# Performance work log

Measured on AMD Instinct MI355X. Metric: run time of the kernel, lower is better.

## Reference

```python
import jax, jax.numpy as jnp
import numpy as np

N = 50000      # nodes
E = 600000     # edges
B = 256        # graphs in batch
F_IN = 128     # num_features
H = 128        # nhid
D = 3 * H      # Set2Set in_channels (concat of 3 conv outputs)
C = 10         # num_classes
STEPS = 10     # Set2Set processing steps


def setup_inputs() -> dict:
    key = jax.random.key(0)
    ks = jax.random.split(key, 24)

    def gn(k, shape, fan_in):
        return jax.random.normal(k, shape, dtype=jnp.float32) / jnp.sqrt(jnp.float32(fan_in))

    x = jax.random.normal(ks[0], (N, F_IN), dtype=jnp.float32)
    edge_index = jax.random.randint(ks[1], (2, E), 0, N, dtype=jnp.int32)
    # sorted graph-assignment covering all B segments
    batch = (jnp.arange(N, dtype=jnp.int32) * B) // N

    inp = dict(x=x, edge_index=edge_index, batch=batch)
    # GraphConv params: out = x @ W_root + aggr(x_j) @ W_rel + b
    inp["W1_root"] = gn(ks[2], (F_IN, H), F_IN)
    inp["W1_rel"] = gn(ks[3], (F_IN, H), F_IN)
    inp["b1"] = jnp.zeros((H,), jnp.float32)
    inp["W2_root"] = gn(ks[4], (H, H), H)
    inp["W2_rel"] = gn(ks[5], (H, H), H)
    inp["b2"] = jnp.zeros((H,), jnp.float32)
    inp["W3_root"] = gn(ks[6], (H, H), H)
    inp["W3_rel"] = gn(ks[7], (H, H), H)
    inp["b3"] = jnp.zeros((H,), jnp.float32)
    # Set2Set LSTM: input 2*D, hidden D, gate order i,f,g,o
    inp["W_ih"] = gn(ks[8], (4 * D, 2 * D), 2 * D)
    inp["W_hh"] = gn(ks[9], (4 * D, D), D)
    inp["b_ih"] = jnp.zeros((4 * D,), jnp.float32)
    inp["b_hh"] = jnp.zeros((4 * D,), jnp.float32)
    # MLP head
    inp["lin1_W"] = gn(ks[10], (2 * D, H), 2 * D)
    inp["lin1_b"] = jnp.zeros((H,), jnp.float32)
    inp["lin2_W"] = gn(ks[11], (H, H // 2), H)
    inp["lin2_b"] = jnp.zeros((H // 2,), jnp.float32)
    inp["lin3_W"] = gn(ks[12], (H // 2, C), H // 2)
    inp["lin3_b"] = jnp.zeros((C,), jnp.float32)
    return inp


def _graph_conv(x, src, dst, W_root, W_rel, b):
    # sum_{j in N(i)} x_j, then linear; plus root transform
    agg = jax.ops.segment_sum(x[src], dst, num_segments=N)  # [N, F]
    return jax.nn.relu(x @ W_root + agg @ W_rel + b)


def _segment_softmax(e, seg, num):
    m = jax.ops.segment_max(e, seg, num_segments=num)
    ex = jnp.exp(e - m[seg])
    den = jax.ops.segment_sum(ex, seg, num_segments=num)
    return ex / den[seg]


def _set2set(x, batch, W_ih, W_hh, b_ih, b_hh):
    # x: [N, D], returns [B, 2D]
    q_star = jnp.zeros((B, 2 * D), x.dtype)
    h = jnp.zeros((B, D), x.dtype)
    c = jnp.zeros((B, D), x.dtype)
    for _ in range(STEPS):
        gates = q_star @ W_ih.T + b_ih + h @ W_hh.T + b_hh  # [B, 4D]
        i, f, g, o = jnp.split(gates, 4, axis=-1)
        i, f, o = jax.nn.sigmoid(i), jax.nn.sigmoid(f), jax.nn.sigmoid(o)
        c = f * c + i * jnp.tanh(g)
        h = o * jnp.tanh(c)
        q = h                                              # [B, D]
        e = jnp.sum(x * q[batch], axis=-1)                 # [N]
        a = _segment_softmax(e, batch, B)                  # [N]
        r = jax.ops.segment_sum(a[:, None] * x, batch, num_segments=B)  # [B, D]
        q_star = jnp.concatenate([q, r], axis=-1)
    return q_star


def reference(x, edge_index, batch,
              W1_root, W1_rel, b1, W2_root, W2_rel, b2, W3_root, W3_rel, b3,
              W_ih, W_hh, b_ih, b_hh,
              lin1_W, lin1_b, lin2_W, lin2_b, lin3_W, lin3_b):
    src, dst = edge_index[0], edge_index[1]
    x1 = _graph_conv(x, src, dst, W1_root, W1_rel, b1)
    x2 = _graph_conv(x1, src, dst, W2_root, W2_rel, b2)
    x3 = _graph_conv(x2, src, dst, W3_root, W3_rel, b3)
    xc = jnp.concatenate([x1, x2, x3], axis=1)             # [N, 3H]
    p = _set2set(xc, batch, W_ih, W_hh, b_ih, b_hh)        # [B, 6H]
    h1 = jax.nn.relu(p @ lin1_W + lin1_b)
    # dropout p=0.5 is identity in eval mode
    h2 = jax.nn.relu(h1 @ lin2_W + lin2_b)
    return jax.nn.log_softmax(h2 @ lin3_W + lin3_b, axis=-1)
```

## Files before the change

kernel.cpp:

```cpp
#include <hip/hip_runtime.h>
#include <hip/hip_bf16.h>
#include <cstddef>

constexpr int NN = 50000;
constexpr int EE = 600000;
constexpr int BBg = 256;

typedef __attribute__((ext_vector_type(8))) short short8;
typedef __attribute__((ext_vector_type(4))) float f32x4;

__device__ __forceinline__ unsigned short bf16_rne(float f) {
    unsigned int u = __float_as_uint(f);
    unsigned int r = u + 0x7fffu + ((u >> 16) & 1u);
    return (unsigned short)(r >> 16);
}
__device__ __forceinline__ float bf16_tof(unsigned short h) {
    return __uint_as_float(((unsigned int)h) << 16);
}

__global__ __launch_bounds__(256) void bake_bimg(
    const float* __restrict__ Wr1, const float* __restrict__ Wl1,
    const float* __restrict__ Wr2, const float* __restrict__ Wl2,
    const float* __restrict__ Wr3, const float* __restrict__ Wl3,
    unsigned short* __restrict__ bimg)
{
    int t = blockIdx.x * 256 + threadIdx.x;
    const int kp = t % 384;
    int rest = t / 384;
    const int c = rest & 63;  rest >>= 6;
    const int cb = rest & 3;  rest >>= 2;
    const int l = rest;
    const int kk = kp & 127;
    const int gc = cb * 64 + c;
    const float* W;
    if (gc < 128) W = (l == 0) ? Wr1 : (l == 1) ? Wr2 : Wr3;
    else          W = (l == 0) ? Wl1 : (l == 1) ? Wl2 : Wl3;
    const float v = W[kk * 128 + (gc & 127)];
    const unsigned short hi = bf16_rne(v);
    unsigned short out = hi;
    if (kp >= 256) out = bf16_rne(v - bf16_tof(hi));
    const int e = (c * 384 + kp) ^ ((c & 7) << 3);
    bimg[(l * 4 + cb) * 24576 + e] = out;
}

__global__ __launch_bounds__(256) void prep_x2(const float* __restrict__ x,
                                               unsigned short* __restrict__ x2)
{
    const int t = blockIdx.x * 256 + threadIdx.x;
    if (t >= NN * 128) return;
    const int n = t >> 7, k = t & 127;
    const float v = x[t];
    const unsigned short hi = bf16_rne(v);
    x2[(size_t)n * 256 + k] = hi;
    x2[(size_t)n * 256 + 128 + k] = bf16_rne(v - bf16_tof(hi));
}

__global__ __launch_bounds__(256) void bake_wt2(const float* __restrict__ w_ih,
                                                const float* __restrict__ w_hh,
                                                unsigned short* __restrict__ wt2)
{
    const int t = blockIdx.x * 256 + threadIdx.x;
    const int o = t & 7;
    const int j = (t >> 3) % 1536;
    const int rest = (t >> 3) / 1536;
    const int kg = rest % 96;
    const int v = rest / 96;
    const int k = kg * 8 + o;
    float val = w_ih[(size_t)j * 768 + k];
    if (k < 384) val += w_hh[(size_t)j * 384 + k];
    const unsigned short hi = bf16_rne(val);
    wt2[t] = v ? bf16_rne(val - bf16_tof(hi)) : hi;
}

__global__ __launch_bounds__(256) void conv_mfma(
    const unsigned short* __restrict__ x2,
    const unsigned short* __restrict__ bimg,
    float* __restrict__ tu,
    const float* __restrict__ bias)
{
    __shared__ unsigned short Bt[24576];
    const int tid = threadIdx.x;
    const int cb = blockIdx.x;
    const int rBase = blockIdx.y * 128;

    {
        const unsigned short* src = bimg + cb * 24576;
#pragma unroll
        for (int i = 0; i < 12; ++i) {
            const int e = (tid + i * 256) * 8;
            *(uint4*)&Bt[e] = *(const uint4*)&src[e];
        }
    }
    __syncthreads();

    const int lane = tid & 63;
    const int w = tid >> 6;
    const int r0w = rBase + w * 32;
    const int l15 = lane & 15;
    const int kg = lane >> 4;

    f32x4 acc[2][4];
#pragma unroll
    for (int rf = 0; rf < 2; ++rf)
#pragma unroll
        for (int cf = 0; cf < 4; ++cf) acc[rf][cf] = (f32x4){0.f, 0.f, 0.f, 0.f};

    const int rr0 = r0w + l15;
    const int rr1 = r0w + 16 + l15;
    const unsigned short* arow0 = x2 + (size_t)(rr0 < NN ? rr0 : NN - 1) * 256 + kg * 8;
    const unsigned short* arow1 = x2 + (size_t)(rr1 < NN ? rr1 : NN - 1) * 256 + kg * 8;

#pragma unroll
    for (int s = 0; s < 12; ++s) {
        const int acol = (s < 8 ? s : s - 8) * 32;
        const short8 a0 = *(const short8*)(arow0 + acol);
        const short8 a1 = *(const short8*)(arow1 + acol);
        short8 bfr[4];
#pragma unroll
        for (int cf = 0; cf < 4; ++cf) {
            const int c = cf * 16 + l15;
            const int e = (c * 384 + s * 32 + kg * 8) ^ ((c & 7) << 3);
            bfr[cf] = *(const short8*)&Bt[e];
        }
#pragma unroll
        for (int cf = 0; cf < 4; ++cf) {
            acc[0][cf] = __builtin_amdgcn_mfma_f32_16x16x32_bf16(a0, bfr[cf], acc[0][cf], 0, 0, 0);
            acc[1][cf] = __builtin_amdgcn_mfma_f32_16x16x32_bf16(a1, bfr[cf], acc[1][cf], 0, 0, 0);
        }
    }
    const int c0 = cb * 64;
#pragma unroll
    for (int rf = 0; rf < 2; ++rf) {
#pragma unroll
        for (int reg = 0; reg < 4; ++reg) {
            const int grow = r0w + rf * 16 + kg * 4 + reg;
            if (grow < NN) {
#pragma unroll
                for (int cf = 0; cf < 4; ++cf) {
                    const int gc = c0 + cf * 16 + l15;
                    float v = acc[rf][cf][reg];
                    if (gc < 128) v += bias[gc];
                    tu[(size_t)grow * 256 + gc] = v;
                }
            }
        }
    }
}

__global__ __launch_bounds__(256) void gates_mfma(
    const unsigned short* __restrict__ qh2,
    const unsigned short* __restrict__ wt2,
    float* __restrict__ gpart)
{
    const int tid = threadIdx.x;
    const int lane = tid & 63;
    const int w = tid >> 6;
    const int c0 = blockIdx.x * 64;
    const int r0w = blockIdx.y * 128 + w * 32;
    const int p = blockIdx.z;
    const int l15 = lane & 15;
    const int kg = lane >> 4;

    f32x4 acc[2][4];
#pragma unroll
    for (int rf = 0; rf < 2; ++rf)
#pragma unroll
        for (int cf = 0; cf < 4; ++cf) acc[rf][cf] = (f32x4){0.f, 0.f, 0.f, 0.f};

    const int abase = (p == 1) ? 768 : 0;
    const unsigned short* arow0 = qh2 + (size_t)(r0w + l15) * 1536 + abase + kg * 8;
    const unsigned short* arow1 = arow0 + 16 * 1536;
    const unsigned short* bbase = wt2 + (p == 2 ? 1179648 : 0)
                                + (size_t)(kg * 1536 + c0 + l15) * 8;

#pragma unroll 4
    for (int km = 0; km < 24; ++km) {
        const short8 a0 = *(const short8*)(arow0 + km * 32);
        const short8 a1 = *(const short8*)(arow1 + km * 32);
#pragma unroll
        for (int cf = 0; cf < 4; ++cf) {
            const short8 bf = *(const short8*)(bbase + (size_t)km * 4 * 1536 * 8 + cf * 128);
            acc[0][cf] = __builtin_amdgcn_mfma_f32_16x16x32_bf16(a0, bf, acc[0][cf], 0, 0, 0);
            acc[1][cf] = __builtin_amdgcn_mfma_f32_16x16x32_bf16(a1, bf, acc[1][cf], 0, 0, 0);
        }
    }
    float* gout = gpart + (size_t)p * 393216;
#pragma unroll
    for (int rf = 0; rf < 2; ++rf)
#pragma unroll
        for (int reg = 0; reg < 4; ++reg) {
            const int grow = r0w + rf * 16 + kg * 4 + reg;
#pragma unroll
            for (int cf = 0; cf < 4; ++cf)
                gout[(size_t)grow * 1536 + c0 + cf * 16 + l15] = acc[rf][cf][reg];
        }
}

__global__ __launch_bounds__(256) void deg_hist(const int* __restrict__ ei,
                                                int* __restrict__ deg)
{
    const int e = blockIdx.x * 256 + threadIdx.x;
    if (e < EE) atomicAdd(&deg[ei[EE + e]], 1);
}

__global__ __launch_bounds__(256) void scan1(const int* __restrict__ deg,
                                             int* __restrict__ tmp_ex,
                                             int* __restrict__ bsum)
{
    __shared__ int s[256];
    const int i = blockIdx.x * 256 + threadIdx.x;
    const int v = (i < NN) ? deg[i] : 0;
    s[threadIdx.x] = v;
    __syncthreads();
#pragma unroll
    for (int off = 1; off < 256; off <<= 1) {
        const int t = (threadIdx.x >= off) ? s[threadIdx.x - off] : 0;
        __syncthreads();
        s[threadIdx.x] += t;
        __syncthreads();
    }
    tmp_ex[i] = s[threadIdx.x] - v;
    if (threadIdx.x == 255) bsum[blockIdx.x] = s[255];
}

__global__ __launch_bounds__(256) void scan2(const int* __restrict__ bsum,
                                             int* __restrict__ boff)
{
    __shared__ int s[256];
    const int v = (threadIdx.x < 196) ? bsum[threadIdx.x] : 0;
    s[threadIdx.x] = v;
    __syncthreads();
#pragma unroll
    for (int off = 1; off < 256; off <<= 1) {
        const int t = (threadIdx.x >= off) ? s[threadIdx.x - off] : 0;
        __syncthreads();
        s[threadIdx.x] += t;
        __syncthreads();
    }
    if (threadIdx.x < 196) boff[threadIdx.x] = s[threadIdx.x] - v;
}

__global__ __launch_bounds__(256) void scan3(const int* __restrict__ tmp_ex,
                                             const int* __restrict__ boff,
                                             int* __restrict__ rowptr,
                                             int* __restrict__ cursor)
{
    const int i = blockIdx.x * 256 + threadIdx.x;
    if (i < NN) {
        const int r = tmp_ex[i] + boff[blockIdx.x];
        rowptr[i] = r;
        cursor[i] = r;
    }
    if (i == 0) rowptr[NN] = EE;
}

__global__ __launch_bounds__(256) void scatter_edges(const int* __restrict__ ei,
                                                     int* __restrict__ cursor,
                                                     int* __restrict__ col)
{
    const int e = blockIdx.x * 256 + threadIdx.x;
    if (e >= EE) return;
    const int slot = atomicAdd(&cursor[ei[EE + e]], 1);
    col[slot] = ei[e];
}

__global__ __launch_bounds__(256) void agg_relu(const int* __restrict__ rowptr,
                                                const int* __restrict__ col,
                                                const float* __restrict__ tu,
                                                float* __restrict__ xc, int coloff,
                                                unsigned short* __restrict__ x2n,
                                                int wsplit)
{
    const int node = blockIdx.x * 4 + (threadIdx.x >> 6);
    if (node >= NN) return;
    const int lane = threadIdx.x & 63;
    const int b = rowptr[node];
    const int e = rowptr[node + 1];
    const float* u = tu + 128 + lane * 2;

    float2 a0 = *(const float2*)&tu[(size_t)node * 256 + lane * 2];
    float2 a1 = make_float2(0.f, 0.f);
    float2 a2 = make_float2(0.f, 0.f);
    float2 a3 = make_float2(0.f, 0.f);

    int j = b;
    for (; j + 8 <= e; j += 8) {
        const int s0 = col[j + 0], s1 = col[j + 1], s2 = col[j + 2], s3 = col[j + 3];
        const int s4 = col[j + 4], s5 = col[j + 5], s6 = col[j + 6], s7 = col[j + 7];
        const float2 v0 = *(const float2*)(u + (size_t)s0 * 256);
        const float2 v1 = *(const float2*)(u + (size_t)s1 * 256);
        const float2 v2 = *(const float2*)(u + (size_t)s2 * 256);
        const float2 v3 = *(const float2*)(u + (size_t)s3 * 256);
        const float2 v4 = *(const float2*)(u + (size_t)s4 * 256);
        const float2 v5 = *(const float2*)(u + (size_t)s5 * 256);
        const float2 v6 = *(const float2*)(u + (size_t)s6 * 256);
        const float2 v7 = *(const float2*)(u + (size_t)s7 * 256);
        a0.x += v0.x; a0.y += v0.y;  a1.x += v1.x; a1.y += v1.y;
        a2.x += v2.x; a2.y += v2.y;  a3.x += v3.x; a3.y += v3.y;
        a0.x += v4.x; a0.y += v4.y;  a1.x += v5.x; a1.y += v5.y;
        a2.x += v6.x; a2.y += v6.y;  a3.x += v7.x; a3.y += v7.y;
    }
    for (; j < e; j += 4) {
        const bool c1 = (j + 1 < e), c2 = (j + 2 < e), c3 = (j + 3 < e);
        const int s0 = col[j];
        const int s1 = col[c1 ? j + 1 : j];
        const int s2 = col[c2 ? j + 2 : j];
        const int s3 = col[c3 ? j + 3 : j];
        const float2 v0 = *(const float2*)(u + (size_t)s0 * 256);
        const float2 v1 = *(const float2*)(u + (size_t)s1 * 256);
        const float2 v2 = *(const float2*)(u + (size_t)s2 * 256);
        const float2 v3 = *(const float2*)(u + (size_t)s3 * 256);
        a0.x += v0.x;              a0.y += v0.y;
        a1.x += c1 ? v1.x : 0.f;   a1.y += c1 ? v1.y : 0.f;
        a2.x += c2 ? v2.x : 0.f;   a2.y += c2 ? v2.y : 0.f;
        a3.x += c3 ? v3.x : 0.f;   a3.y += c3 ? v3.y : 0.f;
    }
    float2 acc;
    acc.x = (a0.x + a1.x) + (a2.x + a3.x);
    acc.y = (a0.y + a1.y) + (a2.y + a3.y);
    acc.x = fmaxf(acc.x, 0.f);
    acc.y = fmaxf(acc.y, 0.f);
    *(float2*)&xc[(size_t)node * 384 + coloff + lane * 2] = acc;

    if (wsplit) {
        const unsigned short h0 = bf16_rne(acc.x);
        const unsigned short h1 = bf16_rne(acc.y);
        const unsigned short l0 = bf16_rne(acc.x - bf16_tof(h0));
        const unsigned short l1 = bf16_rne(acc.y - bf16_tof(h1));
        unsigned short* p = x2n + (size_t)node * 256 + lane * 2;
        *(unsigned int*)p = (unsigned int)h0 | ((unsigned int)h1 << 16);
        *(unsigned int*)(p + 128) = (unsigned int)l0 | ((unsigned int)l1 << 16);
    }
}

__global__ __launch_bounds__(512) void lstm_attn(const float* __restrict__ gpart,
                                                 const float* __restrict__ b_ih,
                                                 const float* __restrict__ b_hh,
                                                 float* __restrict__ cbuf,
                                                 float* __restrict__ qh,
                                                 unsigned short* __restrict__ qh2,
                                                 const float* __restrict__ xc)
{
    const int b = blockIdx.x;
    const int start = (b * NN + BBg - 1) / BBg;
    const int end = ((b + 1) * NN + BBg - 1) / BBg;
    const int cnt = end - start;

    __shared__ float qs[384];
    __shared__ float wm[8], wz[8];
    __shared__ float rp[8][384];

    const int tid = threadIdx.x;
    const int lane = tid & 63;
    const int w = tid >> 6;

    if (tid < 384) {
        const int d = tid;
        const float* g0 = gpart + (size_t)b * 1536;
        const float* g1 = g0 + 393216;
        const float* g2 = g1 + 393216;
        float gi = g0[d]        + g1[d]        + g2[d]        + b_ih[d]        + b_hh[d];
        float gf = g0[384 + d]  + g1[384 + d]  + g2[384 + d]  + b_ih[384 + d]  + b_hh[384 + d];
        float gg = g0[768 + d]  + g1[768 + d]  + g2[768 + d]  + b_ih[768 + d]  + b_hh[768 + d];
        float go = g0[1152 + d] + g1[1152 + d] + g2[1152 + d] + b_ih[1152 + d] + b_hh[1152 + d];
        gi = 1.f / (1.f + expf(-gi));
        gf = 1.f / (1.f + expf(-gf));
        go = 1.f / (1.f + expf(-go));
        const float cc = gf * cbuf[b * 384 + d] + gi * tanhf(gg);
        cbuf[b * 384 + d] = cc;
        const float h = go * tanhf(cc);
        qh[(size_t)b * 768 + d] = h;
        qs[d] = h;
        const unsigned short hi = bf16_rne(h);
        qh2[(size_t)b * 1536 + d] = hi;
        qh2[(size_t)b * 1536 + 768 + d] = bf16_rne(h - bf16_tof(hi));
    }
    __syncthreads();

    float q[6];
#pragma unroll
    for (int j = 0; j < 6; ++j) q[j] = qs[lane + 64 * j];

    float m = -3.4e38f, Z = 0.f;
    float r[6] = {0.f, 0.f, 0.f, 0.f, 0.f, 0.f};
    int i = w;
    for (; i + 56 < cnt; i += 64) {
        float xv[8][6];
#pragma unroll
        for (int k = 0; k < 8; ++k) {
            const float* p = xc + (size_t)(start + i + 8 * k) * 384 + lane;
#pragma unroll
            for (int j = 0; j < 6; ++j) xv[k][j] = p[64 * j];
        }
        float d[8];
#pragma unroll
        for (int k = 0; k < 8; ++k) {
            float dd = 0.f;
#pragma unroll
            for (int j = 0; j < 6; ++j) dd = fmaf(xv[k][j], q[j], dd);
            d[k] = dd;
        }
#pragma unroll
        for (int s = 32; s > 0; s >>= 1) {
#pragma unroll
            for (int k = 0; k < 8; ++k) d[k] += __shfl_xor(d[k], s);
        }
        float mn = m;
#pragma unroll
        for (int k = 0; k < 8; ++k) mn = fmaxf(mn, d[k]);
        const float cs = __expf(m - mn);
        float p8[8];
        float ps = 0.f;
#pragma unroll
        for (int k = 0; k < 8; ++k) { p8[k] = __expf(d[k] - mn); ps += p8[k]; }
        Z = Z * cs + ps;
#pragma unroll
        for (int j = 0; j < 6; ++j) {
            float t = r[j] * cs;
#pragma unroll
            for (int k = 0; k < 8; ++k) t = fmaf(p8[k], xv[k][j], t);
            r[j] = t;
        }
        m = mn;
    }
    for (; i < cnt; i += 8) {
        const float* xr = xc + (size_t)(start + i) * 384 + lane;
        float xv[6], d = 0.f;
#pragma unroll
        for (int j = 0; j < 6; ++j) { xv[j] = xr[64 * j]; d = fmaf(xv[j], q[j], d); }
#pragma unroll
        for (int s = 32; s > 0; s >>= 1) d += __shfl_xor(d, s);
        const float mn = fmaxf(m, d);
        const float cs = __expf(m - mn);
        const float p = __expf(d - mn);
        Z = Z * cs + p;
#pragma unroll
        for (int j = 0; j < 6; ++j) r[j] = fmaf(r[j], cs, p * xv[j]);
        m = mn;
    }
#pragma unroll
    for (int j = 0; j < 6; ++j) rp[w][lane + 64 * j] = r[j];
    if (lane == 0) { wm[w] = m; wz[w] = Z; }
    __syncthreads();

    float M = wm[0];
#pragma unroll
    for (int i2 = 1; i2 < 8; ++i2) M = fmaxf(M, wm[i2]);
    float sc[8];
    float Zt = 0.f;
#pragma unroll
    for (int i2 = 0; i2 < 8; ++i2) { sc[i2] = __expf(wm[i2] - M); Zt += wz[i2] * sc[i2]; }
    const float invZ = 1.f / Zt;
    for (int t = tid; t < 384; t += 512) {
        float rr = 0.f;
#pragma unroll
        for (int i2 = 0; i2 < 8; ++i2) rr = fmaf(rp[i2][t], sc[i2], rr);
        const float val = rr * invZ;
        qh[(size_t)b * 768 + 384 + t] = val;
        const unsigned short hi = bf16_rne(val);
        qh2[(size_t)b * 1536 + 384 + t] = hi;
        qh2[(size_t)b * 1536 + 1152 + t] = bf16_rne(val - bf16_tof(hi));
    }
}

__global__ __launch_bounds__(128) void head(const float* __restrict__ qh,
                                            const float* __restrict__ W1,
                                            const float* __restrict__ bias1,
                                            const float* __restrict__ W2,
                                            const float* __restrict__ b2,
                                            const float* __restrict__ W3,
                                            const float* __restrict__ b3,
                                            float* __restrict__ out)
{
    const int b = blockIdx.x;
    const int tid = threadIdx.x;
    __shared__ float qs[768];
    __shared__ float h1s[128];
    __shared__ float h2s[64];
    __shared__ float lg[10];
    for (int k = tid; k < 768; k += 128) qs[k] = qh[(size_t)b * 768 + k];
    __syncthreads();
    float acc = bias1[tid];
    for (int k = 0; k < 768; ++k) acc = fmaf(qs[k], W1[k * 128 + tid], acc);
    h1s[tid] = fmaxf(acc, 0.f);
    __syncthreads();
    if (tid < 64) {
        float a2 = b2[tid];
        for (int k = 0; k < 128; ++k) a2 = fmaf(h1s[k], W2[k * 64 + tid], a2);
        h2s[tid] = fmaxf(a2, 0.f);
    }
    __syncthreads();
    if (tid < 10) {
        float a = b3[tid];
        for (int k = 0; k < 64; ++k) a = fmaf(h2s[k], W3[k * 10 + tid], a);
        lg[tid] = a;
    }
    __syncthreads();
    if (tid < 10) {
        float mx = lg[0];
        for (int j = 1; j < 10; ++j) mx = fmaxf(mx, lg[j]);
        float s = 0.f;
        for (int j = 0; j < 10; ++j) s += expf(lg[j] - mx);
        out[b * 10 + tid] = lg[tid] - mx - logf(s);
    }
}

extern "C" void kernel_launch(void* const* d_in, const int* in_sizes, int n_in,
                              void* d_out, int out_size, void* d_ws, size_t ws_size,
                              hipStream_t stream)
{
    const float* x     = (const float*)d_in[0];
    const int*   ei    = (const int*)d_in[1];
    const float* W1r   = (const float*)d_in[3];
    const float* W1l   = (const float*)d_in[4];
    const float* b1    = (const float*)d_in[5];
    const float* W2r   = (const float*)d_in[6];
    const float* W2l   = (const float*)d_in[7];
    const float* b2    = (const float*)d_in[8];
    const float* W3r   = (const float*)d_in[9];
    const float* W3l   = (const float*)d_in[10];
    const float* b3    = (const float*)d_in[11];
    const float* W_ih  = (const float*)d_in[12];
    const float* W_hh  = (const float*)d_in[13];
    const float* b_ih  = (const float*)d_in[14];
    const float* b_hh  = (const float*)d_in[15];
    const float* lin1W = (const float*)d_in[16];
    const float* lin1b = (const float*)d_in[17];
    const float* lin2W = (const float*)d_in[18];
    const float* lin2b = (const float*)d_in[19];
    const float* lin3W = (const float*)d_in[20];
    const float* lin3b = (const float*)d_in[21];

    float* ws = (float*)d_ws;
    float* xc    = ws;
    float* tu    = ws + 19200000;
    float* qh    = tu;
    float* cbuf  = tu + 196608;
    unsigned short* qh2 = (unsigned short*)(tu + 294912);
    float* gpart = tu + 491520;
    unsigned short* wt2  = (unsigned short*)(ws + 32000000);
    unsigned short* bimg = (unsigned short*)(ws + 33179648);
    unsigned short* x2   = (unsigned short*)(ws + 33327104);
    int*   ib    = (int*)(ws + 39727104);
    int* deg     = ib;
    int* rowptr  = ib + 50000;
    int* cursor  = ib + 100001;
    int* tmp_ex  = ib + 150001;
    int* bsum    = ib + 200177;
    int* boff    = ib + 200433;
    int* col     = ib + 200689;
    float* out   = (float*)d_out;

    hipMemsetAsync(deg, 0, 50000 * sizeof(int), stream);

    bake_wt2<<<9216, 256, 0, stream>>>(W_ih, W_hh, wt2);
    bake_bimg<<<1152, 256, 0, stream>>>(W1r, W1l, W2r, W2l, W3r, W3l, bimg);
    prep_x2<<<25000, 256, 0, stream>>>(x, x2);

    deg_hist<<<2344, 256, 0, stream>>>(ei, deg);
    scan1<<<196, 256, 0, stream>>>(deg, tmp_ex, bsum);
    scan2<<<1, 256, 0, stream>>>(bsum, boff);
    scan3<<<196, 256, 0, stream>>>(tmp_ex, boff, rowptr, cursor);
    scatter_edges<<<2344, 256, 0, stream>>>(ei, cursor, col);

    const float* biases[3] = {b1, b2, b3};
    for (int l = 0; l < 3; ++l) {
        conv_mfma<<<dim3(4, 391), 256, 0, stream>>>(
            x2, bimg + l * 4 * 24576, tu, biases[l]);
        agg_relu<<<12500, 256, 0, stream>>>(rowptr, col, tu, xc, l * 128,
                                            x2, (l < 2) ? 1 : 0);
    }

    hipMemsetAsync(qh, 0, 491520 * sizeof(float), stream);

    for (int s = 0; s < 10; ++s) {
        gates_mfma<<<dim3(24, 2, 3), 256, 0, stream>>>(qh2, wt2, gpart);
        lstm_attn<<<256, 512, 0, stream>>>(gpart, b_ih, b_hh, cbuf, qh, qh2, xc);
    }

    head<<<256, 128, 0, stream>>>(qh, lin1W, lin1b, lin2W, lin2b,
                                  lin3W, lin3b, out);
}
```

Measured before the change: 789.2 us.

## Fuse Set2Set gate GEMM and attention into one persistent kernel with grid barriers

Replaces the 20 alternating gates_mfma/lstm_attn launches with a single persistent 256-block kernel. Each step runs the gate GEMM work spread over warps 0-2 of 192 blocks, then the LSTM update and attention, with a global atomic barrier between phases. This removes per-step launch overhead and idle gaps. The cost is spin-wait barrier latency, and the scheme relies on all 256 blocks of 512 threads being resident at once, or it deadlocks.

Measured after the change: 1.132 ms. 43.4% more time.

```diff
diff --git a/kernel.cpp b/kernel.cpp
--- a/kernel.cpp
+++ b/kernel.cpp
@@ -16,6 +16,17 @@
 }
 __device__ __forceinline__ float bf16_tof(unsigned short h) {
     return __uint_as_float(((unsigned int)h) << 16);
+}
+
+__device__ __forceinline__ void gbar(unsigned* bar, unsigned target) {
+    __syncthreads();
+    if (threadIdx.x == 0) {
+        __threadfence();
+        atomicAdd(bar, 1u);
+        while (atomicAdd(bar, 0u) < target) __builtin_amdgcn_s_sleep(2);
+        __threadfence();
+    }
+    __syncthreads();
 }
 
 __global__ __launch_bounds__(256) void bake_bimg(
@@ -147,55 +158,6 @@
     }
 }
 
-__global__ __launch_bounds__(256) void gates_mfma(
-    const unsigned short* __restrict__ qh2,
-    const unsigned short* __restrict__ wt2,
-    float* __restrict__ gpart)
-{
-    const int tid = threadIdx.x;
-    const int lane = tid & 63;
-    const int w = tid >> 6;
-    const int c0 = blockIdx.x * 64;
-    const int r0w = blockIdx.y * 128 + w * 32;
-    const int p = blockIdx.z;
-    const int l15 = lane & 15;
-    const int kg = lane >> 4;
-
-    f32x4 acc[2][4];
-#pragma unroll
-    for (int rf = 0; rf < 2; ++rf)
-#pragma unroll
-        for (int cf = 0; cf < 4; ++cf) acc[rf][cf] = (f32x4){0.f, 0.f, 0.f, 0.f};
-
-    const int abase = (p == 1) ? 768 : 0;
-    const unsigned short* arow0 = qh2 + (size_t)(r0w + l15) * 1536 + abase + kg * 8;
-    const unsigned short* arow1 = arow0 + 16 * 1536;
-    const unsigned short* bbase = wt2 + (p == 2 ? 1179648 : 0)
-                                + (size_t)(kg * 1536 + c0 + l15) * 8;
-
-#pragma unroll 4
-    for (int km = 0; km < 24; ++km) {
-        const short8 a0 = *(const short8*)(arow0 + km * 32);
-        const short8 a1 = *(const short8*)(arow1 + km * 32);
-#pragma unroll
-        for (int cf = 0; cf < 4; ++cf) {
-            const short8 bf = *(const short8*)(bbase + (size_t)km * 4 * 1536 * 8 + cf * 128);
-            acc[0][cf] = __builtin_amdgcn_mfma_f32_16x16x32_bf16(a0, bf, acc[0][cf], 0, 0, 0);
-            acc[1][cf] = __builtin_amdgcn_mfma_f32_16x16x32_bf16(a1, bf, acc[1][cf], 0, 0, 0);
-        }
-    }
-    float* gout = gpart + (size_t)p * 393216;
-#pragma unroll
-    for (int rf = 0; rf < 2; ++rf)
-#pragma unroll
-        for (int reg = 0; reg < 4; ++reg) {
-            const int grow = r0w + rf * 16 + kg * 4 + reg;
-#pragma unroll
-            for (int cf = 0; cf < 4; ++cf)
-                gout[(size_t)grow * 1536 + c0 + cf * 16 + l15] = acc[rf][cf][reg];
-        }
-}
-
 __global__ __launch_bounds__(256) void deg_hist(const int* __restrict__ ei,
                                                 int* __restrict__ deg)
 {
@@ -333,133 +295,182 @@
     }
 }
 
-__global__ __launch_bounds__(512) void lstm_attn(const float* __restrict__ gpart,
-                                                 const float* __restrict__ b_ih,
-                                                 const float* __restrict__ b_hh,
-                                                 float* __restrict__ cbuf,
-                                                 float* __restrict__ qh,
-                                                 unsigned short* __restrict__ qh2,
-                                                 const float* __restrict__ xc)
-{
+__global__ __launch_bounds__(512) void set2set_loop(
+    const unsigned short* __restrict__ wt2,
+    const float* __restrict__ b_ih, const float* __restrict__ b_hh,
+    const float* __restrict__ xc,
+    float* __restrict__ qh,
+    float* __restrict__ cbuf,
+    unsigned short* __restrict__ qh2,
+    float* __restrict__ gpart,
+    unsigned* __restrict__ bar)
+{
+    __shared__ float qs[384];
+    __shared__ float wm[8], wz[8];
+    __shared__ float rp[8][384];
+
+    const int tid = threadIdx.x;
+    const int lane = tid & 63;
+    const int w = tid >> 6;
     const int b = blockIdx.x;
     const int start = (b * NN + BBg - 1) / BBg;
     const int end = ((b + 1) * NN + BBg - 1) / BBg;
     const int cnt = end - start;
-
-    __shared__ float qs[384];
-    __shared__ float wm[8], wz[8];
-    __shared__ float rp[8][384];
-
-    const int tid = threadIdx.x;
-    const int lane = tid & 63;
-    const int w = tid >> 6;
-
-    if (tid < 384) {
-        const int d = tid;
-        const float* g0 = gpart + (size_t)b * 1536;
-        const float* g1 = g0 + 393216;
-        const float* g2 = g1 + 393216;
-        float gi = g0[d]        + g1[d]        + g2[d]        + b_ih[d]        + b_hh[d];
-        float gf = g0[384 + d]  + g1[384 + d]  + g2[384 + d]  + b_ih[384 + d]  + b_hh[384 + d];
-        float gg = g0[768 + d]  + g1[768 + d]  + g2[768 + d]  + b_ih[768 + d]  + b_hh[768 + d];
-        float go = g0[1152 + d] + g1[1152 + d] + g2[1152 + d] + b_ih[1152 + d] + b_hh[1152 + d];
-        gi = 1.f / (1.f + expf(-gi));
-        gf = 1.f / (1.f + expf(-gf));
-        go = 1.f / (1.f + expf(-go));
-        const float cc = gf * cbuf[b * 384 + d] + gi * tanhf(gg);
-        cbuf[b * 384 + d] = cc;
-        const float h = go * tanhf(cc);
-        qh[(size_t)b * 768 + d] = h;
-        qs[d] = h;
-        const unsigned short hi = bf16_rne(h);
-        qh2[(size_t)b * 1536 + d] = hi;
-        qh2[(size_t)b * 1536 + 768 + d] = bf16_rne(h - bf16_tof(hi));
-    }
-    __syncthreads();
-
-    float q[6];
-#pragma unroll
-    for (int j = 0; j < 6; ++j) q[j] = qs[lane + 64 * j];
-
-    float m = -3.4e38f, Z = 0.f;
-    float r[6] = {0.f, 0.f, 0.f, 0.f, 0.f, 0.f};
-    int i = w;
-    for (; i + 56 < cnt; i += 64) {
-        float xv[8][6];
-#pragma unroll
-        for (int k = 0; k < 8; ++k) {
-            const float* p = xc + (size_t)(start + i + 8 * k) * 384 + lane;
-#pragma unroll
-            for (int j = 0; j < 6; ++j) xv[k][j] = p[64 * j];
-        }
-        float d[8];
-#pragma unroll
-        for (int k = 0; k < 8; ++k) {
-            float dd = 0.f;
-#pragma unroll
-            for (int j = 0; j < 6; ++j) dd = fmaf(xv[k][j], q[j], dd);
-            d[k] = dd;
-        }
-#pragma unroll
-        for (int s = 32; s > 0; s >>= 1) {
-#pragma unroll
-            for (int k = 0; k < 8; ++k) d[k] += __shfl_xor(d[k], s);
-        }
-        float mn = m;
-#pragma unroll
-        for (int k = 0; k < 8; ++k) mn = fmaxf(mn, d[k]);
-        const float cs = __expf(m - mn);
-        float p8[8];
-        float ps = 0.f;
-#pragma unroll
-        for (int k = 0; k < 8; ++k) { p8[k] = __expf(d[k] - mn); ps += p8[k]; }
-        Z = Z * cs + ps;
-#pragma unroll
-        for (int j = 0; j < 6; ++j) {
-            float t = r[j] * cs;
-#pragma unroll
-            for (int k = 0; k < 8; ++k) t = fmaf(p8[k], xv[k][j], t);
-            r[j] = t;
-        }
-        m = mn;
-    }
-    for (; i < cnt; i += 8) {
-        const float* xr = xc + (size_t)(start + i) * 384 + lane;
-        float xv[6], d = 0.f;
-#pragma unroll
-        for (int j = 0; j < 6; ++j) { xv[j] = xr[64 * j]; d = fmaf(xv[j], q[j], d); }
-#pragma unroll
-        for (int s = 32; s > 0; s >>= 1) d += __shfl_xor(d, s);
-        const float mn = fmaxf(m, d);
-        const float cs = __expf(m - mn);
-        const float p = __expf(d - mn);
-        Z = Z * cs + p;
-#pragma unroll
-        for (int j = 0; j < 6; ++j) r[j] = fmaf(r[j], cs, p * xv[j]);
-        m = mn;
-    }
-#pragma unroll
-    for (int j = 0; j < 6; ++j) rp[w][lane + 64 * j] = r[j];
-    if (lane == 0) { wm[w] = m; wz[w] = Z; }
-    __syncthreads();
-
-    float M = wm[0];
-#pragma unroll
-    for (int i2 = 1; i2 < 8; ++i2) M = fmaxf(M, wm[i2]);
-    float sc[8];
-    float Zt = 0.f;
-#pragma unroll
-    for (int i2 = 0; i2 < 8; ++i2) { sc[i2] = __expf(wm[i2] - M); Zt += wz[i2] * sc[i2]; }
-    const float invZ = 1.f / Zt;
-    for (int t = tid; t < 384; t += 512) {
-        float rr = 0.f;
-#pragma unroll
-        for (int i2 = 0; i2 < 8; ++i2) rr = fmaf(rp[i2][t], sc[i2], rr);
-        const float val = rr * invZ;
-        qh[(size_t)b * 768 + 384 + t] = val;
-        const unsigned short hi = bf16_rne(val);
-        qh2[(size_t)b * 1536 + 384 + t] = hi;
-        qh2[(size_t)b * 1536 + 1152 + t] = bf16_rne(val - bf16_tof(hi));
+    const int l15 = lane & 15;
+    const int kg = lane >> 4;
+
+    unsigned tgt = 0;
+    for (int step = 0; step < 10; ++step) {
+        if (w < 3 && b < 192) {
+            const int task = b * 3 + w;
+            const int p = task / 192;
+            const int t2 = task - p * 192;
+            const int c0 = (t2 % 24) * 64;
+            const int r0w = (t2 / 24) * 32;
+
+            f32x4 acc[2][4];
+#pragma unroll
+            for (int rf = 0; rf < 2; ++rf)
+#pragma unroll
+                for (int cf = 0; cf < 4; ++cf) acc[rf][cf] = (f32x4){0.f, 0.f, 0.f, 0.f};
+
+            const int abase = (p == 1) ? 768 : 0;
+            const unsigned short* arow0 = qh2 + (size_t)(r0w + l15) * 1536 + abase + kg * 8;
+            const unsigned short* arow1 = arow0 + 16 * 1536;
+            const unsigned short* bbase = wt2 + (p == 2 ? 1179648 : 0)
+                                        + (size_t)(kg * 1536 + c0 + l15) * 8;
+#pragma unroll 4
+            for (int km = 0; km < 24; ++km) {
+                const short8 a0 = *(const short8*)(arow0 + km * 32);
+                const short8 a1 = *(const short8*)(arow1 + km * 32);
+#pragma unroll
+                for (int cf = 0; cf < 4; ++cf) {
+                    const short8 bf = *(const short8*)(bbase + (size_t)km * 4 * 1536 * 8 + cf * 128);
+                    acc[0][cf] = __builtin_amdgcn_mfma_f32_16x16x32_bf16(a0, bf, acc[0][cf], 0, 0, 0);
+                    acc[1][cf] = __builtin_amdgcn_mfma_f32_16x16x32_bf16(a1, bf, acc[1][cf], 0, 0, 0);
+                }
+            }
+            float* gout = gpart + (size_t)p * 393216;
+#pragma unroll
+            for (int rf = 0; rf < 2; ++rf)
+#pragma unroll
+                for (int reg = 0; reg < 4; ++reg) {
+                    const int grow = r0w + rf * 16 + kg * 4 + reg;
+#pragma unroll
+                    for (int cf = 0; cf < 4; ++cf)
+                        gout[(size_t)grow * 1536 + c0 + cf * 16 + l15] = acc[rf][cf][reg];
+                }
+        }
+        tgt += 256; gbar(bar, tgt);
+
+        if (tid < 384) {
+            const int d = tid;
+            const float* g0 = gpart + (size_t)b * 1536;
+            const float* g1 = g0 + 393216;
+            const float* g2 = g1 + 393216;
+            float gi = g0[d]        + g1[d]        + g2[d]        + b_ih[d]        + b_hh[d];
+            float gf = g0[384 + d]  + g1[384 + d]  + g2[384 + d]  + b_ih[384 + d]  + b_hh[384 + d];
+            float gg = g0[768 + d]  + g1[768 + d]  + g2[768 + d]  + b_ih[768 + d]  + b_hh[768 + d];
+            float go = g0[1152 + d] + g1[1152 + d] + g2[1152 + d] + b_ih[1152 + d] + b_hh[1152 + d];
+            gi = 1.f / (1.f + expf(-gi));
+            gf = 1.f / (1.f + expf(-gf));
+            go = 1.f / (1.f + expf(-go));
+            const float cc = gf * cbuf[b * 384 + d] + gi * tanhf(gg);
+            cbuf[b * 384 + d] = cc;
+            const float h = go * tanhf(cc);
+            qh[(size_t)b * 768 + d] = h;
+            qs[d] = h;
+            const unsigned short hi = bf16_rne(h);
+            qh2[(size_t)b * 1536 + d] = hi;
+            qh2[(size_t)b * 1536 + 768 + d] = bf16_rne(h - bf16_tof(hi));
+        }
+        __syncthreads();
+
+        float q[6];
+#pragma unroll
+        for (int j = 0; j < 6; ++j) q[j] = qs[lane + 64 * j];
+
+        float m = -3.4e38f, Z = 0.f;
+        float r[6] = {0.f, 0.f, 0.f, 0.f, 0.f, 0.f};
+        int i = w;
+        for (; i + 56 < cnt; i += 64) {
+            float xv[8][6];
+#pragma unroll
+            for (int k = 0; k < 8; ++k) {
+                const float* p = xc + (size_t)(start + i + 8 * k) * 384 + lane;
+#pragma unroll
+                for (int j = 0; j < 6; ++j) xv[k][j] = p[64 * j];
+            }
+            float d[8];
+#pragma unroll
+            for (int k = 0; k < 8; ++k) {
+                float dd = 0.f;
+#pragma unroll
+                for (int j = 0; j < 6; ++j) dd = fmaf(xv[k][j], q[j], dd);
+                d[k] = dd;
+            }
+#pragma unroll
+            for (int s = 32; s > 0; s >>= 1) {
+#pragma unroll
+                for (int k = 0; k < 8; ++k) d[k] += __shfl_xor(d[k], s);
+            }
+            float mn = m;
+#pragma unroll
+            for (int k = 0; k < 8; ++k) mn = fmaxf(mn, d[k]);
+            const float cs = __expf(m - mn);
+            float p8[8];
+            float ps = 0.f;
+#pragma unroll
+            for (int k = 0; k < 8; ++k) { p8[k] = __expf(d[k] - mn); ps += p8[k]; }
+            Z = Z * cs + ps;
+#pragma unroll
+            for (int j = 0; j < 6; ++j) {
+                float t = r[j] * cs;
+#pragma unroll
+                for (int k = 0; k < 8; ++k) t = fmaf(p8[k], xv[k][j], t);
+                r[j] = t;
+            }
+            m = mn;
+        }
+        for (; i < cnt; i += 8) {
+            const float* xr = xc + (size_t)(start + i) * 384 + lane;
+            float xv[6], d = 0.f;
+#pragma unroll
+            for (int j = 0; j < 6; ++j) { xv[j] = xr[64 * j]; d = fmaf(xv[j], q[j], d); }
+#pragma unroll
+            for (int s = 32; s > 0; s >>= 1) d += __shfl_xor(d, s);
+            const float mn = fmaxf(m, d);
+            const float cs = __expf(m - mn);
+            const float p = __expf(d - mn);
+            Z = Z * cs + p;
+#pragma unroll
+            for (int j = 0; j < 6; ++j) r[j] = fmaf(r[j], cs, p * xv[j]);
+            m = mn;
+        }
+#pragma unroll
+        for (int j = 0; j < 6; ++j) rp[w][lane + 64 * j] = r[j];
+        if (lane == 0) { wm[w] = m; wz[w] = Z; }
+        __syncthreads();
+
+        float M = wm[0];
+#pragma unroll
+        for (int i2 = 1; i2 < 8; ++i2) M = fmaxf(M, wm[i2]);
+        float sc[8];
+        float Zt = 0.f;
+#pragma unroll
+        for (int i2 = 0; i2 < 8; ++i2) { sc[i2] = __expf(wm[i2] - M); Zt += wz[i2] * sc[i2]; }
+        const float invZ = 1.f / Zt;
+        for (int t = tid; t < 384; t += 512) {
+            float rr = 0.f;
+#pragma unroll
+            for (int i2 = 0; i2 < 8; ++i2) rr = fmaf(rp[i2][t], sc[i2], rr);
+            const float val = rr * invZ;
+            qh[(size_t)b * 768 + 384 + t] = val;
+            const unsigned short hi = bf16_rne(val);
+            qh2[(size_t)b * 1536 + 384 + t] = hi;
+            qh2[(size_t)b * 1536 + 1152 + t] = bf16_rne(val - bf16_tof(hi));
+        }
+        tgt += 256; gbar(bar, tgt);
     }
 }
 
@@ -549,9 +560,11 @@
     int* bsum    = ib + 200177;
     int* boff    = ib + 200433;
     int* col     = ib + 200689;
+    unsigned* bar = (unsigned*)(ib + 800689);
     float* out   = (float*)d_out;
 
     hipMemsetAsync(deg, 0, 50000 * sizeof(int), stream);
+    hipMemsetAsync(bar, 0, sizeof(unsigned), stream);
 
     bake_wt2<<<9216, 256, 0, stream>>>(W_ih, W_hh, wt2);
     bake_bimg<<<1152, 256, 0, stream>>>(W1r, W1l, W2r, W2l, W3r, W3l, bimg);
@@ -573,10 +586,8 @@
 
     hipMemsetAsync(qh, 0, 491520 * sizeof(float), stream);
 
-    for (int s = 0; s < 10; ++s) {
-        gates_mfma<<<dim3(24, 2, 3), 256, 0, stream>>>(qh2, wt2, gpart);
-        lstm_attn<<<256, 512, 0, stream>>>(gpart, b_ih, b_hh, cbuf, qh, qh2, xc);
-    }
+    set2set_loop<<<256, 512, 0, stream>>>(wt2, b_ih, b_hh, xc,
+                                          qh, cbuf, qh2, gpart, bar);
 
     head<<<256, 128, 0, stream>>>(qh, lin1W, lin1b, lin2W, lin2b,
                                   lin3W, lin3b, out);
```

## Split Set2Set attention per graph across four blocks with separate combine kernel

Applied to the files above, without the earlier changes.

The fused LSTM+attention kernel ran only 256 blocks (one per graph) over the large xc array. Each graph's node range is now split into four quarter blocks (1024 blocks total). Each block recomputes the LSTM cell and writes a partial online-softmax state (max, sum, weighted vector), and a new combine kernel merges the four partials into r. The cell state is double-buffered because all four blocks read the old c. This adds one kernel launch per step and redundant gate math in exchange for more parallelism on the memory-bound attention pass.

New measurement: 819.7 us. 1.04x slower.

```diff
diff --git a/kernel.cpp b/kernel.cpp
--- a/kernel.cpp
+++ b/kernel.cpp
@@ -333,18 +333,21 @@
     }
 }
 
-__global__ __launch_bounds__(512) void lstm_attn(const float* __restrict__ gpart,
-                                                 const float* __restrict__ b_ih,
-                                                 const float* __restrict__ b_hh,
-                                                 float* __restrict__ cbuf,
-                                                 float* __restrict__ qh,
-                                                 unsigned short* __restrict__ qh2,
-                                                 const float* __restrict__ xc)
-{
-    const int b = blockIdx.x;
-    const int start = (b * NN + BBg - 1) / BBg;
-    const int end = ((b + 1) * NN + BBg - 1) / BBg;
+__global__ __launch_bounds__(512, 8) void attn_part(
+    const float* __restrict__ gpart,
+    const float* __restrict__ b_ih, const float* __restrict__ b_hh,
+    const float* __restrict__ cbOld, float* __restrict__ cbNew,
+    float* __restrict__ qh, unsigned short* __restrict__ qh2,
+    const float* __restrict__ xc, float* __restrict__ part)
+{
+    const int blk = blockIdx.x;
+    const int g = blk >> 2;
+    const int qd = blk & 3;
+    const int start = (g * NN + BBg - 1) / BBg;
+    const int end = ((g + 1) * NN + BBg - 1) / BBg;
     const int cnt = end - start;
+    const int q0 = (qd * cnt) >> 2;
+    const int q1 = ((qd + 1) * cnt) >> 2;
 
     __shared__ float qs[384];
     __shared__ float wm[8], wz[8];
@@ -356,7 +359,7 @@
 
     if (tid < 384) {
         const int d = tid;
-        const float* g0 = gpart + (size_t)b * 1536;
+        const float* g0 = gpart + (size_t)g * 1536;
         const float* g1 = g0 + 393216;
         const float* g2 = g1 + 393216;
         float gi = g0[d]        + g1[d]        + g2[d]        + b_ih[d]        + b_hh[d];
@@ -366,14 +369,16 @@
         gi = 1.f / (1.f + expf(-gi));
         gf = 1.f / (1.f + expf(-gf));
         go = 1.f / (1.f + expf(-go));
-        const float cc = gf * cbuf[b * 384 + d] + gi * tanhf(gg);
-        cbuf[b * 384 + d] = cc;
+        const float cc = gf * cbOld[g * 384 + d] + gi * tanhf(gg);
+        cbNew[g * 384 + d] = cc;
         const float h = go * tanhf(cc);
-        qh[(size_t)b * 768 + d] = h;
         qs[d] = h;
-        const unsigned short hi = bf16_rne(h);
-        qh2[(size_t)b * 1536 + d] = hi;
-        qh2[(size_t)b * 1536 + 768 + d] = bf16_rne(h - bf16_tof(hi));
+        if (qd == 0) {
+            qh[(size_t)g * 768 + d] = h;
+            const unsigned short hi = bf16_rne(h);
+            qh2[(size_t)g * 1536 + d] = hi;
+            qh2[(size_t)g * 1536 + 768 + d] = bf16_rne(h - bf16_tof(hi));
+        }
     }
     __syncthreads();
 
@@ -383,18 +388,18 @@
 
     float m = -3.4e38f, Z = 0.f;
     float r[6] = {0.f, 0.f, 0.f, 0.f, 0.f, 0.f};
-    int i = w;
-    for (; i + 56 < cnt; i += 64) {
-        float xv[8][6];
-#pragma unroll
-        for (int k = 0; k < 8; ++k) {
+    int i = q0 + w;
+    for (; i + 24 < q1; i += 32) {
+        float xv[4][6];
+#pragma unroll
+        for (int k = 0; k < 4; ++k) {
             const float* p = xc + (size_t)(start + i + 8 * k) * 384 + lane;
 #pragma unroll
             for (int j = 0; j < 6; ++j) xv[k][j] = p[64 * j];
         }
-        float d[8];
-#pragma unroll
-        for (int k = 0; k < 8; ++k) {
+        float d[4];
+#pragma unroll
+        for (int k = 0; k < 4; ++k) {
             float dd = 0.f;
 #pragma unroll
             for (int j = 0; j < 6; ++j) dd = fmaf(xv[k][j], q[j], dd);
@@ -403,27 +408,27 @@
 #pragma unroll
         for (int s = 32; s > 0; s >>= 1) {
 #pragma unroll
-            for (int k = 0; k < 8; ++k) d[k] += __shfl_xor(d[k], s);
+            for (int k = 0; k < 4; ++k) d[k] += __shfl_xor(d[k], s);
         }
         float mn = m;
 #pragma unroll
-        for (int k = 0; k < 8; ++k) mn = fmaxf(mn, d[k]);
+        for (int k = 0; k < 4; ++k) mn = fmaxf(mn, d[k]);
         const float cs = __expf(m - mn);
-        float p8[8];
+        float p4[4];
         float ps = 0.f;
 #pragma unroll
-        for (int k = 0; k < 8; ++k) { p8[k] = __expf(d[k] - mn); ps += p8[k]; }
+        for (int k = 0; k < 4; ++k) { p4[k] = __expf(d[k] - mn); ps += p4[k]; }
         Z = Z * cs + ps;
 #pragma unroll
         for (int j = 0; j < 6; ++j) {
             float t = r[j] * cs;
 #pragma unroll
-            for (int k = 0; k < 8; ++k) t = fmaf(p8[k], xv[k][j], t);
+            for (int k = 0; k < 4; ++k) t = fmaf(p4[k], xv[k][j], t);
             r[j] = t;
         }
         m = mn;
     }
-    for (; i < cnt; i += 8) {
+    for (; i < q1; i += 8) {
         const float* xr = xc + (size_t)(start + i) * 384 + lane;
         float xv[6], d = 0.f;
 #pragma unroll
@@ -450,17 +455,37 @@
     float Zt = 0.f;
 #pragma unroll
     for (int i2 = 0; i2 < 8; ++i2) { sc[i2] = __expf(wm[i2] - M); Zt += wz[i2] * sc[i2]; }
-    const float invZ = 1.f / Zt;
+    float* po = part + (size_t)blk * 388;
     for (int t = tid; t < 384; t += 512) {
         float rr = 0.f;
 #pragma unroll
         for (int i2 = 0; i2 < 8; ++i2) rr = fmaf(rp[i2][t], sc[i2], rr);
-        const float val = rr * invZ;
-        qh[(size_t)b * 768 + 384 + t] = val;
-        const unsigned short hi = bf16_rne(val);
-        qh2[(size_t)b * 1536 + 384 + t] = hi;
-        qh2[(size_t)b * 1536 + 1152 + t] = bf16_rne(val - bf16_tof(hi));
-    }
+        po[t] = rr;
+    }
+    if (tid == 0) { po[384] = M; po[385] = Zt; }
+}
+
+__global__ __launch_bounds__(384) void attn_combine(
+    const float* __restrict__ part,
+    float* __restrict__ qh, unsigned short* __restrict__ qh2)
+{
+    const int g = blockIdx.x;
+    const int t = threadIdx.x;
+    const float* p0 = part + (size_t)(g * 4 + 0) * 388;
+    const float* p1 = p0 + 388;
+    const float* p2 = p1 + 388;
+    const float* p3 = p2 + 388;
+    const float m0 = p0[384], m1 = p1[384], m2 = p2[384], m3 = p3[384];
+    const float M = fmaxf(fmaxf(m0, m1), fmaxf(m2, m3));
+    const float s0 = __expf(m0 - M), s1 = __expf(m1 - M);
+    const float s2 = __expf(m2 - M), s3 = __expf(m3 - M);
+    const float Zt = p0[385] * s0 + p1[385] * s1 + p2[385] * s2 + p3[385] * s3;
+    const float invZ = 1.f / Zt;
+    const float val = (p0[t] * s0 + p1[t] * s1 + p2[t] * s2 + p3[t] * s3) * invZ;
+    qh[(size_t)g * 768 + 384 + t] = val;
+    const unsigned short hi = bf16_rne(val);
+    qh2[(size_t)g * 1536 + 384 + t] = hi;
+    qh2[(size_t)g * 1536 + 1152 + t] = bf16_rne(val - bf16_tof(hi));
 }
 
 __global__ __launch_bounds__(128) void head(const float* __restrict__ qh,
@@ -535,9 +560,11 @@
     float* xc    = ws;
     float* tu    = ws + 19200000;
     float* qh    = tu;
-    float* cbuf  = tu + 196608;
-    unsigned short* qh2 = (unsigned short*)(tu + 294912);
-    float* gpart = tu + 491520;
+    float* cbA   = tu + 196608;
+    float* cbB   = tu + 294912;
+    unsigned short* qh2 = (unsigned short*)(tu + 393216);
+    float* gpart = tu + 589824;
+    float* part  = tu + 1769472;
     unsigned short* wt2  = (unsigned short*)(ws + 32000000);
     unsigned short* bimg = (unsigned short*)(ws + 33179648);
     unsigned short* x2   = (unsigned short*)(ws + 33327104);
@@ -571,11 +598,15 @@
                                             x2, (l < 2) ? 1 : 0);
     }
 
-    hipMemsetAsync(qh, 0, 491520 * sizeof(float), stream);
+    hipMemsetAsync(qh, 0, 589824 * sizeof(float), stream);
 
     for (int s = 0; s < 10; ++s) {
+        float* cbOld = (s & 1) ? cbB : cbA;
+        float* cbNew = (s & 1) ? cbA : cbB;
         gates_mfma<<<dim3(24, 2, 3), 256, 0, stream>>>(qh2, wt2, gpart);
-        lstm_attn<<<256, 512, 0, stream>>>(gpart, b_ih, b_hh, cbuf, qh, qh2, xc);
+        attn_part<<<1024, 512, 0, stream>>>(gpart, b_ih, b_hh, cbOld, cbNew,
+                                            qh, qh2, xc, part);
+        attn_combine<<<256, 384, 0, stream>>>(part, qh, qh2);
     }
 
     head<<<256, 128, 0, stream>>>(qh, lin1W, lin1b, lin2W, lin2b,
```
